# Kernel optimization log

Hardware: AMD Instinct MI355X
Metric: run time of the kernel (lower is better)

The kernel has to match this reference:

```python
import jax, jax.numpy as jnp
import numpy as np

N_T = 100  # number of time grid points for the ODE solve, matching torch.linspace(0, 1, 100)


def setup_inputs() -> dict:
    key = jax.random.key(0)
    kx, kw, kb, kc, kd = jax.random.split(key, 5)
    H = 1024
    N = 16384
    return {
        "x": jax.random.normal(kx, (N, H), dtype=jnp.float32),
        "W": jax.random.normal(kw, (H, H), dtype=jnp.float32),
        "b": jax.random.normal(kb, (H,), dtype=jnp.float32),
        "c": jax.random.normal(kc, (H,), dtype=jnp.float32),
        "d": jax.random.normal(kd, (H,), dtype=jnp.float32),
    }


def reference(x, W, b, c, d):
    # fused matmul + trig elementwise: z = x @ W + b*sin(x) + c*cos(x) + d*tan(x)
    z = jnp.matmul(x, W) + b * jnp.sin(x) + c * jnp.cos(x) + d * jnp.tan(x)

    # ODE: dy/dt = -y + t*z, y(0)=0, integrated on linspace(0,1,100), return y(1).
    ts = jnp.linspace(0.0, 1.0, N_T, dtype=z.dtype)
    t0 = ts[:-1]
    dts = ts[1:] - ts[:-1]

    def f(t, y):
        return -y + t * z

    def rk4_step(y, t_dt):
        t, dt = t_dt
        k1 = f(t, y)
        k2 = f(t + 0.5 * dt, y + 0.5 * dt * k1)
        k3 = f(t + 0.5 * dt, y + 0.5 * dt * k2)
        k4 = f(t + dt, y + dt * k3)
        y_next = y + (dt / 6.0) * (k1 + 2.0 * k2 + 2.0 * k3 + k4)
        return y_next, None

    y0 = jnp.zeros_like(z)
    y_final, _ = jax.lax.scan(rk4_step, y0, (t0, dts))
    return y_final
```

## Files before the change

kernel.cpp:

```cpp
#include <hip/hip_runtime.h>
#include <hip/hip_bf16.h>

typedef __attribute__((ext_vector_type(4))) float  f32x4;
typedef __attribute__((ext_vector_type(8))) short  bf16x8;
typedef __attribute__((ext_vector_type(4))) short  bf16x4v;

#define EPAD 68
#define AS1 __attribute__((address_space(1)))
#define AS3 __attribute__((address_space(3)))

__device__ __forceinline__ unsigned short f2bf(float f) {
  __hip_bfloat16 h = __float2bfloat16(f);
  unsigned short u; __builtin_memcpy(&u, &h, 2); return u;
}
__device__ __forceinline__ float bf2f(short u) {
  unsigned int w = ((unsigned int)(unsigned short)u) << 16;
  float f; __builtin_memcpy(&f, &w, 4); return f;
}

__device__ __forceinline__ void my_sincos(float xf, float& s_out, float& c_out) {
  const float kf = __builtin_rintf(xf * 0.636619772367581343f);
  const int   q  = (int)kf;
  const double kd = (double)kf;
  double rd = __builtin_fma(-kd, 1.5707963267948966,    (double)xf);
  rd        = __builtin_fma(-kd, 6.123233995736766e-17, rd);
  const float r = (float)rd;
  const float z = r * r;
  const float ps = fmaf(z, fmaf(z, fmaf(z, 2.7183114939898219e-06f,
                                           -1.9839334836096632e-04f),
                                   8.3333293858894632e-03f),
                        -1.6666666641626524e-01f);
  const float sr = fmaf(r * z, ps, r);
  const float pc = fmaf(z, fmaf(z, fmaf(z, 2.4390448796277409e-05f,
                                           -1.3886763774609929e-03f),
                                   4.1666623323739063e-02f),
                        -4.9999999725103100e-01f);
  const float cr = fmaf(z, pc, 1.0f);
  const bool swap = (q & 1) != 0;
  float s1 = swap ? cr : sr;
  float c1 = swap ? sr : cr;
  if (q & 2)       s1 = -s1;
  if ((q + 1) & 2) c1 = -c1;
  s_out = s1; c_out = c1;
}

__global__ __launch_bounds__(256)
void prep_all(const float* __restrict__ W, const float* __restrict__ x,
              const float* __restrict__ bv, const float* __restrict__ cv,
              const float* __restrict__ dv,
              unsigned short* __restrict__ Wt, unsigned short* __restrict__ xb,
              unsigned short* __restrict__ g, int H, int n4) {
  __shared__ float tile[64][65];
  const int t = threadIdx.x;
  if (blockIdx.x < 256) {
    const int blk = blockIdx.x;
    const int n0 = (blk & 15) << 6;
    const int k0 = (blk >> 4) << 6;
    #pragma unroll
    for (int it = 0; it < 4; ++it) {
      int q = it * 256 + t;
      int r = q >> 4, c4 = (q & 15) << 2;
      f32x4 v = *(const f32x4*)&W[(size_t)(k0 + r) * H + n0 + c4];
      tile[r][c4 + 0] = v[0]; tile[r][c4 + 1] = v[1];
      tile[r][c4 + 2] = v[2]; tile[r][c4 + 3] = v[3];
    }
    __syncthreads();
    #pragma unroll
    for (int it = 0; it < 4; ++it) {
      int q = it * 256 + t;
      int r = q >> 4, c4 = (q & 15) << 2;
      bf16x4v o;
      #pragma unroll
      for (int j = 0; j < 4; ++j) o[j] = (short)f2bf(tile[c4 + j][r]);
      *(bf16x4v*)&Wt[(size_t)(n0 + r) * H + k0 + c4] = o;
    }
  } else {
    const int jm = (H >> 2) - 1;
    int i = (blockIdx.x - 256) * 256 + t;
    const int stride = ((int)gridDim.x - 256) * 256;
    for (; i < n4; i += stride) {
      f32x4 v = ((const f32x4*)x)[i];
      const int j4 = (i & jm) << 2;
      f32x4 b4 = *(const f32x4*)&bv[j4];
      f32x4 c4 = *(const f32x4*)&cv[j4];
      f32x4 d4 = *(const f32x4*)&dv[j4];
      bf16x4v xo, go;
      #pragma unroll
      for (int e = 0; e < 4; ++e) {
        xo[e] = (short)f2bf(v[e]);
        float s, co;
        my_sincos(v[e], s, co);
        const float tn = s * __builtin_amdgcn_rcpf(co);
        go[e] = (short)f2bf(fmaf(b4[e], s, fmaf(c4[e], co, d4[e] * tn)));
      }
      ((bf16x4v*)xb)[i] = xo;
      ((bf16x4v*)g)[i]  = go;
    }
  }
}

__global__ __launch_bounds__(256)
void transpose_W(const float* __restrict__ W, unsigned short* __restrict__ Wt, int H) {
  __shared__ float tile[64][65];
  const int k0 = blockIdx.y * 64;
  const int n0 = blockIdx.x * 64;
  const int t = threadIdx.x;
  #pragma unroll
  for (int it = 0; it < 4; ++it) {
    int q = it * 256 + t;
    int r = q >> 4, c4 = (q & 15) << 2;
    f32x4 v = *(const f32x4*)&W[(size_t)(k0 + r) * H + n0 + c4];
    tile[r][c4 + 0] = v[0]; tile[r][c4 + 1] = v[1];
    tile[r][c4 + 2] = v[2]; tile[r][c4 + 3] = v[3];
  }
  __syncthreads();
  #pragma unroll
  for (int it = 0; it < 4; ++it) {
    int q = it * 256 + t;
    int r = q >> 4, c4 = (q & 15) << 2;
    bf16x4v o;
    #pragma unroll
    for (int j = 0; j < 4; ++j) o[j] = (short)f2bf(tile[c4 + j][r]);
    *(bf16x4v*)&Wt[(size_t)(n0 + r) * H + k0 + c4] = o;
  }
}
__global__ __launch_bounds__(256)
void cvt_x(const float* __restrict__ x, unsigned short* __restrict__ xb, int n4) {
  int i = blockIdx.x * 256 + threadIdx.x;
  const int stride = gridDim.x * 256;
  for (; i < n4; i += stride) {
    f32x4 v = ((const f32x4*)x)[i];
    bf16x4v o;
    #pragma unroll
    for (int j = 0; j < 4; ++j) o[j] = (short)f2bf(v[j]);
    ((bf16x4v*)xb)[i] = o;
  }
}

__global__ __launch_bounds__(512, 4)
void gemm_256(const unsigned short* __restrict__ xb,
              const unsigned short* __restrict__ Wt,
              const unsigned short* __restrict__ g,
              float* __restrict__ out, float S, int H) {
  __shared__ unsigned char smem[49152];
  float* Es = (float*)smem;

  const int tid  = threadIdx.x;
  const int nwg  = gridDim.x;
  const int work = (blockIdx.x & 7) * (nwg >> 3) + (blockIdx.x >> 3);
  const int nbj  = H >> 7;
  const int bj   = work % nbj;
  const int bi   = work / nbj;
  const int i0   = bi * 256, j0 = bj * 128;
  const int wave = tid >> 6, lane = tid & 63;
  const int wr   = wave >> 1, wc = wave & 1;
  const int l16  = lane & 15, lq = lane >> 4;

  const unsigned short *aS0, *aS1, *bS0;
  {
    const int D0 = tid * 16,        sup0 = D0 >> 7;
    const int sl0 = ((D0 >> 4) & 7) ^ (sup0 & 7);
    const int r0  = sup0 * 2 + (sl0 >> 2), c0 = (sl0 & 3) << 3;
    const int D1 = 8192 + tid * 16, sup1 = D1 >> 7;
    const int sl1 = ((D1 >> 4) & 7) ^ (sup1 & 7);
    const int r1  = sup1 * 2 + (sl1 >> 2), c1 = (sl1 & 3) << 3;
    aS0 = &xb[(size_t)(i0 + r0) * H + c0];
    aS1 = &xb[(size_t)(i0 + r1) * H + c1];
    bS0 = &Wt[(size_t)(j0 + r0) * H + c0];
  }

  #define STAGE(bufsel, kOff)                                                   \
    do {                                                                        \
      char* _b = (char*)smem + (bufsel) * 24576;                                \
      __builtin_amdgcn_global_load_lds((const AS1 void*)(aS0 + (kOff)),         \
        (AS3 void*)(_b + tid * 16), 16, 0, 0);                                  \
      __builtin_amdgcn_global_load_lds((const AS1 void*)(aS1 + (kOff)),         \
        (AS3 void*)(_b + 8192 + tid * 16), 16, 0, 0);                           \
      __builtin_amdgcn_global_load_lds((const AS1 void*)(bS0 + (kOff)),         \
        (AS3 void*)(_b + 16384 + tid * 16), 16, 0, 0);                          \
    } while (0)

  const int slotx = (4 * (l16 & 1) + lq) ^ ((l16 >> 1) & 7);
  const int laneT = (l16 >> 1) * 128 + slotx * 16;
  const int aBase = wr * 4096 + laneT;
  const int bBase = wc * 4096 + laneT;

  f32x4 acc[4][4] = {};

  const int nsteps = H >> 5;
  STAGE(0, 0);
  __syncthreads();
  for (int t = 0; t < nsteps; ++t) {
    if (t + 1 < nsteps) STAGE((t + 1) & 1, (t + 1) * 32);
    const char* Ab = (const char*)smem + (t & 1) * 24576;
    const char* Bb = Ab + 16384;
    bf16x8 bfr[4];
    #pragma unroll
    for (int ni = 0; ni < 4; ++ni)
      bfr[ni] = *(const bf16x8*)(Bb + bBase + ni * 1024);
    #pragma unroll
    for (int mi = 0; mi < 4; ++mi) {
      bf16x8 af = *(const bf16x8*)(Ab + aBase + mi * 1024);
      #pragma unroll
      for (int ni = 0; ni < 4; ++ni)
        acc[mi][ni] = __builtin_amdgcn_mfma_f32_16x16x32_bf16(af, bfr[ni], acc[mi][ni], 0, 0, 0);
    }
    __syncthreads();
  }
  #undef STAGE

  float* ep = Es + wave * (16 * EPAD);
  const int rr = lane >> 2;
  const int cq = (lane & 3) * 16;
  #pragma unroll
  for (int mi = 0; mi < 4; ++mi) {
    #pragma unroll
    for (int ni = 0; ni < 4; ++ni)
      #pragma unroll
      for (int r = 0; r < 4; ++r)
        ep[(lq * 4 + r) * EPAD + ni * 16 + l16] = acc[mi][ni][r];
    const int i  = i0 + wr * 64 + mi * 16 + rr;
    const int jb = j0 + wc * 64 + cq;
    float* orow = &out[(size_t)i * H + jb];
    const unsigned short* grow = &g[(size_t)i * H + jb];
    #pragma unroll
    for (int t = 0; t < 4; ++t) {
      f32x4 a = *(const f32x4*)&ep[rr * EPAD + cq + 4 * t];
      bf16x4v gv = *(const bf16x4v*)&grow[4 * t];
      f32x4 o;
      #pragma unroll
      for (int e = 0; e < 4; ++e) o[e] = S * (a[e] + bf2f(gv[e]));
      *(f32x4*)&orow[4 * t] = o;
    }
  }
}

template <int MODE>
__global__ __launch_bounds__(256, 2)
void gemm_fb(const float* __restrict__ x, const unsigned short* __restrict__ xb,
             const unsigned short* __restrict__ Wt,
             const float* __restrict__ bv, const float* __restrict__ cv,
             const float* __restrict__ dv, float* __restrict__ out,
             float S, int H) {
  __shared__ unsigned char smem[36864];
  unsigned short* As = (unsigned short*)smem;
  unsigned short* Bs = As + 128 * 72;
  float*          Es = (float*)smem;

  const int tid  = threadIdx.x;
  const int nwg  = gridDim.x;
  const int work = (nwg % 8 == 0) ? (blockIdx.x & 7) * (nwg >> 3) + (blockIdx.x >> 3)
                                  : blockIdx.x;
  const int nbj  = H / 128;
  const int bj   = work % nbj;
  const int bi   = work / nbj;
  const int i0   = bi * 128, j0 = bj * 128;
  const int wave = tid >> 6, lane = tid & 63;
  const int wr = wave >> 1, wc = wave & 1;
  const int l16 = lane & 15, lq = lane >> 4;

  f32x4 acc[4][4] = {};
  for (int kk = 0; kk < H; kk += 64) {
    if constexpr (MODE == 1) {
      #pragma unroll
      for (int it = 0; it < 4; ++it) {
        int q = it * 256 + tid;
        int r = q >> 3, c8 = (q & 7) << 3;
        *(bf16x8*)&As[r * 72 + c8] = *(const bf16x8*)&xb[(size_t)(i0 + r) * H + kk + c8];
      }
    } else {
      #pragma unroll
      for (int it = 0; it < 8; ++it) {
        int q = it * 256 + tid;
        int r = q >> 4, c4 = (q & 15) << 2;
        f32x4 v = *(const f32x4*)&x[(size_t)(i0 + r) * H + kk + c4];
        bf16x4v o;
        #pragma unroll
        for (int j = 0; j < 4; ++j) o[j] = (short)f2bf(v[j]);
        *(bf16x4v*)&As[r * 72 + c4] = o;
      }
    }
    #pragma unroll
    for (int it = 0; it < 4; ++it) {
      int q = it * 256 + tid;
      int r = q >> 3, c8 = (q & 7) << 3;
      *(bf16x8*)&Bs[r * 72 + c8] = *(const bf16x8*)&Wt[(size_t)(j0 + r) * H + kk + c8];
    }
    __syncthreads();
    #pragma unroll
    for (int s = 0; s < 2; ++s) {
      bf16x8 af[4], bfr[4];
      #pragma unroll
      for (int mi = 0; mi < 4; ++mi)
        af[mi] = *(const bf16x8*)&As[(wr * 64 + mi * 16 + l16) * 72 + s * 32 + lq * 8];
      #pragma unroll
      for (int ni = 0; ni < 4; ++ni)
        bfr[ni] = *(const bf16x8*)&Bs[(wc * 64 + ni * 16 + l16) * 72 + s * 32 + lq * 8];
      #pragma unroll
      for (int mi = 0; mi < 4; ++mi)
        #pragma unroll
        for (int ni = 0; ni < 4; ++ni)
          acc[mi][ni] = __builtin_amdgcn_mfma_f32_16x16x32_bf16(af[mi], bfr[ni], acc[mi][ni], 0, 0, 0);
    }
    __syncthreads();
  }
  float* ep = Es + wave * (16 * EPAD);
  const int rr = lane >> 2;
  const int cq = (lane & 3) * 16;
  #pragma unroll
  for (int mi = 0; mi < 4; ++mi) {
    #pragma unroll
    for (int ni = 0; ni < 4; ++ni)
      #pragma unroll
      for (int r = 0; r < 4; ++r)
        ep[(lq * 4 + r) * EPAD + ni * 16 + l16] = acc[mi][ni][r];
    const int i  = i0 + wr * 64 + mi * 16 + rr;
    const int jb = j0 + wc * 64 + cq;
    const float* xrow = &x[(size_t)i * H + jb];
    float*       orow = &out[(size_t)i * H + jb];
    #pragma unroll
    for (int t = 0; t < 4; ++t) {
      f32x4 a  = *(const f32x4*)&ep[rr * EPAD + cq + 4 * t];
      f32x4 xv = *(const f32x4*)&xrow[4 * t];
      f32x4 b4 = *(const f32x4*)&bv[jb + 4 * t];
      f32x4 c4 = *(const f32x4*)&cv[jb + 4 * t];
      f32x4 d4 = *(const f32x4*)&dv[jb + 4 * t];
      f32x4 o;
      #pragma unroll
      for (int e = 0; e < 4; ++e) {
        float s, co;
        my_sincos(xv[e], s, co);
        const float tanv = s * __builtin_amdgcn_rcpf(co);
        o[e] = S * (fmaf(b4[e], s, a[e]) + fmaf(c4[e], co, d4[e] * tanv));
      }
      *(f32x4*)&orow[4 * t] = o;
    }
  }
}

extern "C" void kernel_launch(void* const* d_in, const int* in_sizes, int n_in,
                              void* d_out, int out_size, void* d_ws, size_t ws_size,
                              hipStream_t stream) {
  const float* x = (const float*)d_in[0];
  const float* W = (const float*)d_in[1];
  const float* b = (const float*)d_in[2];
  const float* c = (const float*)d_in[3];
  const float* d = (const float*)d_in[4];
  float* out = (float*)d_out;
  const int H = in_sizes[2];
  const int M = in_sizes[0] / H;

  const int NT = 100;
  float ts[NT];
  const float step = (float)(1.0 / 99.0);
  for (int i = 0; i < NT; ++i) ts[i] = (float)i * step;
  ts[NT - 1] = 1.0f;
  double yy = 0.0;
  for (int i = 0; i < NT - 1; ++i) {
    const double t = (double)ts[i], dt = (double)(ts[i + 1] - ts[i]);
    const double k1 = t - yy;
    const double k2 = (t + 0.5 * dt) - (yy + 0.5 * dt * k1);
    const double k3 = (t + 0.5 * dt) - (yy + 0.5 * dt * k2);
    const double k4 = (t + dt) - (yy + dt * k3);
    yy += dt / 6.0 * (k1 + 2.0 * k2 + 2.0 * k3 + k4);
  }
  const float S = (float)yy;

  unsigned short* Wt = (unsigned short*)d_ws;
  unsigned short* xb = Wt + (size_t)H * H;
  unsigned short* g  = xb + (size_t)M * H;
  const size_t needW  = (size_t)H * H * 2;
  const size_t needXb = (size_t)M * H * 2;
  const int n4 = M * H / 4;

  const int nblk = (M / 256) * (H / 128);
  const bool shapeOK = (H % 128 == 0) && (M % 256 == 0) && (nblk % 8 == 0)
                    && ((H >> 5) >= 2);

  if (ws_size >= needW + 2 * needXb && shapeOK) {
    prep_all<<<256 + 2048, 256, 0, stream>>>(W, x, b, c, d, Wt, xb, g, H, n4);
    gemm_256<<<nblk, 512, 0, stream>>>(xb, Wt, g, out, S, H);
  } else if (ws_size >= needW + needXb) {
    dim3 tgrid(H / 64, H / 64);
    transpose_W<<<tgrid, 256, 0, stream>>>(W, Wt, H);
    cvt_x<<<2048, 256, 0, stream>>>(x, xb, n4);
    gemm_fb<1><<<(H / 128) * (M / 128), 256, 0, stream>>>(x, xb, Wt, b, c, d, out, S, H);
  } else {
    dim3 tgrid(H / 64, H / 64);
    transpose_W<<<tgrid, 256, 0, stream>>>(W, Wt, H);
    gemm_fb<2><<<(H / 128) * (M / 128), 256, 0, stream>>>(x, nullptr, Wt, b, c, d, out, S, H);
  }
}
```

Before: 80.21 us.

## Fuse bf16 conversion and trig epilogue into GEMM, drop prep kernel

New measurement: 76.35 us. 1.05x faster.

```diff
diff --git a/kernel.cpp b/kernel.cpp
--- a/kernel.cpp
+++ b/kernel.cpp
@@ -6,16 +6,10 @@
 typedef __attribute__((ext_vector_type(4))) short  bf16x4v;
 
 #define EPAD 68
-#define AS1 __attribute__((address_space(1)))
-#define AS3 __attribute__((address_space(3)))
 
 __device__ __forceinline__ unsigned short f2bf(float f) {
   __hip_bfloat16 h = __float2bfloat16(f);
   unsigned short u; __builtin_memcpy(&u, &h, 2); return u;
-}
-__device__ __forceinline__ float bf2f(short u) {
-  unsigned int w = ((unsigned int)(unsigned short)u) << 16;
-  float f; __builtin_memcpy(&f, &w, 4); return f;
 }
 
 __device__ __forceinline__ void my_sincos(float xf, float& s_out, float& c_out) {
@@ -44,59 +38,8 @@
   s_out = s1; c_out = c1;
 }
 
-__global__ __launch_bounds__(256)
-void prep_all(const float* __restrict__ W, const float* __restrict__ x,
-              const float* __restrict__ bv, const float* __restrict__ cv,
-              const float* __restrict__ dv,
-              unsigned short* __restrict__ Wt, unsigned short* __restrict__ xb,
-              unsigned short* __restrict__ g, int H, int n4) {
-  __shared__ float tile[64][65];
-  const int t = threadIdx.x;
-  if (blockIdx.x < 256) {
-    const int blk = blockIdx.x;
-    const int n0 = (blk & 15) << 6;
-    const int k0 = (blk >> 4) << 6;
-    #pragma unroll
-    for (int it = 0; it < 4; ++it) {
-      int q = it * 256 + t;
-      int r = q >> 4, c4 = (q & 15) << 2;
-      f32x4 v = *(const f32x4*)&W[(size_t)(k0 + r) * H + n0 + c4];
-      tile[r][c4 + 0] = v[0]; tile[r][c4 + 1] = v[1];
-      tile[r][c4 + 2] = v[2]; tile[r][c4 + 3] = v[3];
-    }
-    __syncthreads();
-    #pragma unroll
-    for (int it = 0; it < 4; ++it) {
-      int q = it * 256 + t;
-      int r = q >> 4, c4 = (q & 15) << 2;
-      bf16x4v o;
-      #pragma unroll
-      for (int j = 0; j < 4; ++j) o[j] = (short)f2bf(tile[c4 + j][r]);
-      *(bf16x4v*)&Wt[(size_t)(n0 + r) * H + k0 + c4] = o;
-    }
-  } else {
-    const int jm = (H >> 2) - 1;
-    int i = (blockIdx.x - 256) * 256 + t;
-    const int stride = ((int)gridDim.x - 256) * 256;
-    for (; i < n4; i += stride) {
-      f32x4 v = ((const f32x4*)x)[i];
-      const int j4 = (i & jm) << 2;
-      f32x4 b4 = *(const f32x4*)&bv[j4];
-      f32x4 c4 = *(const f32x4*)&cv[j4];
-      f32x4 d4 = *(const f32x4*)&dv[j4];
-      bf16x4v xo, go;
-      #pragma unroll
-      for (int e = 0; e < 4; ++e) {
-        xo[e] = (short)f2bf(v[e]);
-        float s, co;
-        my_sincos(v[e], s, co);
-        const float tn = s * __builtin_amdgcn_rcpf(co);
-        go[e] = (short)f2bf(fmaf(b4[e], s, fmaf(c4[e], co, d4[e] * tn)));
-      }
-      ((bf16x4v*)xb)[i] = xo;
-      ((bf16x4v*)g)[i]  = go;
-    }
-  }
+__device__ __forceinline__ int swz(int r, int c) {
+  return (r >> 1) * 128 + (((4 * (r & 1) + c) ^ ((r >> 1) & 7)) << 4);
 }
 
 __global__ __launch_bounds__(256)
@@ -124,24 +67,13 @@
     *(bf16x4v*)&Wt[(size_t)(n0 + r) * H + k0 + c4] = o;
   }
 }
-__global__ __launch_bounds__(256)
-void cvt_x(const float* __restrict__ x, unsigned short* __restrict__ xb, int n4) {
-  int i = blockIdx.x * 256 + threadIdx.x;
-  const int stride = gridDim.x * 256;
-  for (; i < n4; i += stride) {
-    f32x4 v = ((const f32x4*)x)[i];
-    bf16x4v o;
-    #pragma unroll
-    for (int j = 0; j < 4; ++j) o[j] = (short)f2bf(v[j]);
-    ((bf16x4v*)xb)[i] = o;
-  }
-}
 
 __global__ __launch_bounds__(512, 4)
-void gemm_256(const unsigned short* __restrict__ xb,
-              const unsigned short* __restrict__ Wt,
-              const unsigned short* __restrict__ g,
-              float* __restrict__ out, float S, int H) {
+void gemm_fused256(const float* __restrict__ x,
+                   const unsigned short* __restrict__ Wt,
+                   const float* __restrict__ bv, const float* __restrict__ cv,
+                   const float* __restrict__ dv,
+                   float* __restrict__ out, float S, int H) {
   __shared__ unsigned char smem[49152];
   float* Es = (float*)smem;
 
@@ -156,29 +88,16 @@
   const int wr   = wave >> 1, wc = wave & 1;
   const int l16  = lane & 15, lq = lane >> 4;
 
-  const unsigned short *aS0, *aS1, *bS0;
-  {
-    const int D0 = tid * 16,        sup0 = D0 >> 7;
-    const int sl0 = ((D0 >> 4) & 7) ^ (sup0 & 7);
-    const int r0  = sup0 * 2 + (sl0 >> 2), c0 = (sl0 & 3) << 3;
-    const int D1 = 8192 + tid * 16, sup1 = D1 >> 7;
-    const int sl1 = ((D1 >> 4) & 7) ^ (sup1 & 7);
-    const int r1  = sup1 * 2 + (sl1 >> 2), c1 = (sl1 & 3) << 3;
-    aS0 = &xb[(size_t)(i0 + r0) * H + c0];
-    aS1 = &xb[(size_t)(i0 + r1) * H + c1];
-    bS0 = &Wt[(size_t)(j0 + r0) * H + c0];
-  }
-
-  #define STAGE(bufsel, kOff)                                                   \
-    do {                                                                        \
-      char* _b = (char*)smem + (bufsel) * 24576;                                \
-      __builtin_amdgcn_global_load_lds((const AS1 void*)(aS0 + (kOff)),         \
-        (AS3 void*)(_b + tid * 16), 16, 0, 0);                                  \
-      __builtin_amdgcn_global_load_lds((const AS1 void*)(aS1 + (kOff)),         \
-        (AS3 void*)(_b + 8192 + tid * 16), 16, 0, 0);                           \
-      __builtin_amdgcn_global_load_lds((const AS1 void*)(bS0 + (kOff)),         \
-        (AS3 void*)(_b + 16384 + tid * 16), 16, 0, 0);                          \
-    } while (0)
+  const int qa0 = tid,        ra0 = qa0 >> 2, ca0 = (qa0 & 3) << 3;
+  const int qa1 = tid + 512,  ra1 = qa1 >> 2, ca1 = (qa1 & 3) << 3;
+  const int pa0 = swz(ra0, qa0 & 3);
+  const int pa1 = swz(ra1, qa1 & 3);
+  const int rb  = tid >> 2,   cbo = (tid & 3) << 3;
+  const int pb  = swz(rb, tid & 3);
+
+  const float*          aP0 = &x[(size_t)(i0 + ra0) * H + ca0];
+  const float*          aP1 = &x[(size_t)(i0 + ra1) * H + ca1];
+  const unsigned short* bP  = &Wt[(size_t)(j0 + rb) * H + cbo];
 
   const int slotx = (4 * (l16 & 1) + lq) ^ ((l16 >> 1) & 7);
   const int laneT = (l16 >> 1) * 128 + slotx * 16;
@@ -187,27 +106,50 @@
 
   f32x4 acc[4][4] = {};
 
-  const int nsteps = H >> 5;
-  STAGE(0, 0);
-  __syncthreads();
-  for (int t = 0; t < nsteps; ++t) {
-    if (t + 1 < nsteps) STAGE((t + 1) & 1, (t + 1) * 32);
-    const char* Ab = (const char*)smem + (t & 1) * 24576;
-    const char* Bb = Ab + 16384;
-    bf16x8 bfr[4];
-    #pragma unroll
-    for (int ni = 0; ni < 4; ++ni)
-      bfr[ni] = *(const bf16x8*)(Bb + bBase + ni * 1024);
-    #pragma unroll
-    for (int mi = 0; mi < 4; ++mi) {
-      bf16x8 af = *(const bf16x8*)(Ab + aBase + mi * 1024);
+  for (int kk = 0; kk < H; kk += 64) {
+    #pragma unroll
+    for (int s = 0; s < 2; ++s) {
+      const int ko = kk + s * 32;
+      {
+        f32x4 v0 = *(const f32x4*)(aP0 + ko);
+        f32x4 v1 = *(const f32x4*)(aP0 + ko + 4);
+        bf16x8 o;
+        #pragma unroll
+        for (int e = 0; e < 4; ++e) { o[e] = (short)f2bf(v0[e]); o[e + 4] = (short)f2bf(v1[e]); }
+        *(bf16x8*)((char*)smem + s * 16384 + pa0) = o;
+      }
+      {
+        f32x4 v0 = *(const f32x4*)(aP1 + ko);
+        f32x4 v1 = *(const f32x4*)(aP1 + ko + 4);
+        bf16x8 o;
+        #pragma unroll
+        for (int e = 0; e < 4; ++e) { o[e] = (short)f2bf(v0[e]); o[e + 4] = (short)f2bf(v1[e]); }
+        *(bf16x8*)((char*)smem + s * 16384 + pa1) = o;
+      }
+      {
+        bf16x8 w = *(const bf16x8*)(bP + ko);
+        *(bf16x8*)((char*)smem + 32768 + s * 8192 + pb) = w;
+      }
+    }
+    __syncthreads();
+    #pragma unroll
+    for (int s = 0; s < 2; ++s) {
+      const char* Ab = (const char*)smem + s * 16384;
+      const char* Bb = (const char*)smem + 32768 + s * 8192;
+      bf16x8 bfr[4];
       #pragma unroll
       for (int ni = 0; ni < 4; ++ni)
-        acc[mi][ni] = __builtin_amdgcn_mfma_f32_16x16x32_bf16(af, bfr[ni], acc[mi][ni], 0, 0, 0);
+        bfr[ni] = *(const bf16x8*)(Bb + bBase + ni * 1024);
+      #pragma unroll
+      for (int mi = 0; mi < 4; ++mi) {
+        bf16x8 af = *(const bf16x8*)(Ab + aBase + mi * 1024);
+        #pragma unroll
+        for (int ni = 0; ni < 4; ++ni)
+          acc[mi][ni] = __builtin_amdgcn_mfma_f32_16x16x32_bf16(af, bfr[ni], acc[mi][ni], 0, 0, 0);
+      }
     }
     __syncthreads();
   }
-  #undef STAGE
 
   float* ep = Es + wave * (16 * EPAD);
   const int rr = lane >> 2;
@@ -221,24 +163,30 @@
         ep[(lq * 4 + r) * EPAD + ni * 16 + l16] = acc[mi][ni][r];
     const int i  = i0 + wr * 64 + mi * 16 + rr;
     const int jb = j0 + wc * 64 + cq;
-    float* orow = &out[(size_t)i * H + jb];
-    const unsigned short* grow = &g[(size_t)i * H + jb];
+    const float* xrow = &x[(size_t)i * H + jb];
+    float*       orow = &out[(size_t)i * H + jb];
     #pragma unroll
     for (int t = 0; t < 4; ++t) {
-      f32x4 a = *(const f32x4*)&ep[rr * EPAD + cq + 4 * t];
-      bf16x4v gv = *(const bf16x4v*)&grow[4 * t];
+      f32x4 a  = *(const f32x4*)&ep[rr * EPAD + cq + 4 * t];
+      f32x4 xv = *(const f32x4*)&xrow[4 * t];
+      f32x4 b4 = *(const f32x4*)&bv[jb + 4 * t];
+      f32x4 c4 = *(const f32x4*)&cv[jb + 4 * t];
+      f32x4 d4 = *(const f32x4*)&dv[jb + 4 * t];
       f32x4 o;
       #pragma unroll
-      for (int e = 0; e < 4; ++e) o[e] = S * (a[e] + bf2f(gv[e]));
+      for (int e = 0; e < 4; ++e) {
+        float s, co;
+        my_sincos(xv[e], s, co);
+        const float tanv = s * __builtin_amdgcn_rcpf(co);
+        o[e] = S * (fmaf(b4[e], s, a[e]) + fmaf(c4[e], co, d4[e] * tanv));
+      }
       *(f32x4*)&orow[4 * t] = o;
     }
   }
 }
 
-template <int MODE>
 __global__ __launch_bounds__(256, 2)
-void gemm_fb(const float* __restrict__ x, const unsigned short* __restrict__ xb,
-             const unsigned short* __restrict__ Wt,
+void gemm_fb(const float* __restrict__ x, const unsigned short* __restrict__ Wt,
              const float* __restrict__ bv, const float* __restrict__ cv,
              const float* __restrict__ dv, float* __restrict__ out,
              float S, int H) {
@@ -261,24 +209,15 @@
 
   f32x4 acc[4][4] = {};
   for (int kk = 0; kk < H; kk += 64) {
-    if constexpr (MODE == 1) {
-      #pragma unroll
-      for (int it = 0; it < 4; ++it) {
-        int q = it * 256 + tid;
-        int r = q >> 3, c8 = (q & 7) << 3;
-        *(bf16x8*)&As[r * 72 + c8] = *(const bf16x8*)&xb[(size_t)(i0 + r) * H + kk + c8];
-      }
-    } else {
-      #pragma unroll
-      for (int it = 0; it < 8; ++it) {
-        int q = it * 256 + tid;
-        int r = q >> 4, c4 = (q & 15) << 2;
-        f32x4 v = *(const f32x4*)&x[(size_t)(i0 + r) * H + kk + c4];
-        bf16x4v o;
-        #pragma unroll
-        for (int j = 0; j < 4; ++j) o[j] = (short)f2bf(v[j]);
-        *(bf16x4v*)&As[r * 72 + c4] = o;
-      }
+    #pragma unroll
+    for (int it = 0; it < 8; ++it) {
+      int q = it * 256 + tid;
+      int r = q >> 4, c4 = (q & 15) << 2;
+      f32x4 v = *(const f32x4*)&x[(size_t)(i0 + r) * H + kk + c4];
+      bf16x4v o;
+      #pragma unroll
+      for (int j = 0; j < 4; ++j) o[j] = (short)f2bf(v[j]);
+      *(bf16x4v*)&As[r * 72 + c4] = o;
     }
     #pragma unroll
     for (int it = 0; it < 4; ++it) {
@@ -367,27 +306,16 @@
   const float S = (float)yy;
 
   unsigned short* Wt = (unsigned short*)d_ws;
-  unsigned short* xb = Wt + (size_t)H * H;
-  unsigned short* g  = xb + (size_t)M * H;
-  const size_t needW  = (size_t)H * H * 2;
-  const size_t needXb = (size_t)M * H * 2;
-  const int n4 = M * H / 4;
-
   const int nblk = (M / 256) * (H / 128);
   const bool shapeOK = (H % 128 == 0) && (M % 256 == 0) && (nblk % 8 == 0)
-                    && ((H >> 5) >= 2);
-
-  if (ws_size >= needW + 2 * needXb && shapeOK) {
-    prep_all<<<256 + 2048, 256, 0, stream>>>(W, x, b, c, d, Wt, xb, g, H, n4);
-    gemm_256<<<nblk, 512, 0, stream>>>(xb, Wt, g, out, S, H);
-  } else if (ws_size >= needW + needXb) {
-    dim3 tgrid(H / 64, H / 64);
-    transpose_W<<<tgrid, 256, 0, stream>>>(W, Wt, H);
-    cvt_x<<<2048, 256, 0, stream>>>(x, xb, n4);
-    gemm_fb<1><<<(H / 128) * (M / 128), 256, 0, stream>>>(x, xb, Wt, b, c, d, out, S, H);
+                    && (H % 64 == 0);
+
+  dim3 tgrid(H / 64, H / 64);
+  transpose_W<<<tgrid, 256, 0, stream>>>(W, Wt, H);
+
+  if (shapeOK) {
+    gemm_fused256<<<nblk, 512, 0, stream>>>(x, Wt, b, c, d, out, S, H);
   } else {
-    dim3 tgrid(H / 64, H / 64);
-    transpose_W<<<tgrid, 256, 0, stream>>>(W, Wt, H);
-    gemm_fb<2><<<(H / 128) * (M / 128), 256, 0, stream>>>(x, nullptr, Wt, b, c, d, out, S, H);
-  }
-}
+    gemm_fb<<<(H / 128) * (M / 128), 256, 0, stream>>>(x, Wt, b, c, d, out, S, H);
+  }
+}
```
